# Optimization experiments

Hardware: AMD Instinct MI355X
Metric: run time of the kernel (lower is better)

The kernel has to match this reference:

```python
import jax, jax.numpy as jnp
import numpy as np

B, H, W = 16, 512, 512
NF, EMB, HEADS, NCLS, G = 1024, 768, 12, 4, 16

# segment start indices: RL pts 0:44, LL 44:94, heart 94:120 (groups not connected)
_SEG_STARTS = np.concatenate([np.arange(0, 43), np.arange(44, 93), np.arange(94, 119)])
# num_regions==6 ROI boxes mapped to the 16x16 grid: rows int(b0*16):int(b2*16), cols int(b1*16):int(b3*16)
_BOXES = [(0, 6, 0, 8), (4, 11, 0, 8), (9, 16, 0, 8), (0, 6, 8, 16), (4, 11, 8, 16), (9, 16, 8, 16)]


def _rasterize(landmarks):
    # vectorized replacement of the per-point index_put_/arange loops
    pts = jnp.clip((landmarks * H).astype(jnp.int32), 0, H - 1)   # [B,120,2] (x,y)
    p1 = pts[:, _SEG_STARTS]                                      # [B,S,2]
    p2 = pts[:, _SEG_STARTS + 1]
    k = jnp.arange(H)                                             # max steps per segment
    dy = p2[..., 1] - p1[..., 1]
    dx = p2[..., 0] - p1[..., 0]
    valid = (k < dy[..., None]) & (k < dx[..., None])             # [B,S,K]
    yi = jnp.clip(p1[..., 1:2] + k, 0, H - 1)
    xi = jnp.clip(p1[..., 0:1] + k, 0, W - 1)
    b = jnp.arange(landmarks.shape[0])[:, None, None]
    flat = ((b * H + yi) * W + xi).reshape(-1)
    mask = jnp.zeros(landmarks.shape[0] * H * W, jnp.float32)
    mask = mask.at[flat].max(valid.reshape(-1).astype(jnp.float32))
    return mask.reshape(-1, 1, H, W)


def _affine_grid(theta):
    # torch.nn.functional.affine_grid, align_corners=False
    xs = (2.0 * jnp.arange(W) + 1.0) / W - 1.0
    ys = (2.0 * jnp.arange(H) + 1.0) / H - 1.0
    gx, gy = jnp.meshgrid(xs, ys)                                 # [H,W]
    base = jnp.stack([gx, gy, jnp.ones_like(gx)], -1)             # [H,W,3]
    return jnp.einsum('hwk,bjk->bhwj', base, theta)               # [B,H,W,2]


def _grid_sample(img, grid):
    # bilinear, zero padding, align_corners=False
    Bs, C, Hi, Wi = img.shape
    fx = ((grid[..., 0] + 1.0) * Wi - 1.0) * 0.5
    fy = ((grid[..., 1] + 1.0) * Hi - 1.0) * 0.5
    x0, y0 = jnp.floor(fx), jnp.floor(fy)
    wx1, wy1 = fx - x0, fy - y0
    b = jnp.arange(Bs)[:, None, None]

    def gather(yi, xi):
        ok = (yi >= 0) & (yi < Hi) & (xi >= 0) & (xi < Wi)
        v = img[b, :, jnp.clip(yi, 0, Hi - 1).astype(jnp.int32), jnp.clip(xi, 0, Wi - 1).astype(jnp.int32)]  # [B,H,W,C]
        return v * ok[..., None]

    out = (gather(y0, x0) * ((1 - wy1) * (1 - wx1))[..., None]
           + gather(y0, x0 + 1) * ((1 - wy1) * wx1)[..., None]
           + gather(y0 + 1, x0) * (wy1 * (1 - wx1))[..., None]
           + gather(y0 + 1, x0 + 1) * (wy1 * wx1)[..., None])
    return out.transpose(0, 3, 1, 2)


def _ln(x, g, b):
    m = x.mean(-1, keepdims=True)
    v = ((x - m) ** 2).mean(-1, keepdims=True)
    return (x - m) / jnp.sqrt(v + 1e-5) * g + b


def _pool_rois(x):
    outs = [jax.image.resize(x[:, :, r0:r1, c0:c1], (x.shape[0], x.shape[1], G, G), 'bilinear')
            for r0, r1, c0, c1 in _BOXES]
    return jnp.stack(outs, 1)                                     # [B,6,C,16,16]


def _forward(x, landmarks, stn_w1, stn_b1, stn_w2, stn_b2, conv_w, conv_b, pe_w, pe_b, pos,
             ln1_g, ln1_b, qkv_w, qkv_b, proj_w, proj_b, ln2_g, ln2_b,
             mlp_w1, mlp_b1, mlp_w2, mlp_b2, fc_w, fc_b):
    seg_mask = jax.lax.stop_gradient(_rasterize(landmarks))       # frozen no_grad seg path
    # STN localization: pool mask -> dense(50) -> dense(6) affine theta
    pooled = seg_mask.reshape(B, 1, 32, H // 32, 32, W // 32).mean((3, 5))
    h = jnp.tanh(pooled.reshape(B, -1) @ stn_w1 + stn_b1)
    theta = (h @ stn_w2 + stn_b2).reshape(B, 2, 3)
    grid = _affine_grid(theta)
    transformed_mask = _grid_sample(seg_mask, grid)
    transformed_img = _grid_sample(x, grid)
    # backbone stand-in: stride-32 conv 512->16, num_features=1024
    feat = jax.lax.conv_general_dilated(transformed_img, conv_w, (32, 32), 'VALID')
    feat = jax.nn.relu(feat + conv_b[None, :, None, None])        # [B,NF,16,16]
    tok = feat.reshape(B, NF, G * G).transpose(0, 2, 1) @ pe_w + pe_b + pos
    # one pre-norm transformer encoder block
    t = _ln(tok, ln1_g, ln1_b)
    qkv = (t @ qkv_w + qkv_b).reshape(B, G * G, 3, HEADS, EMB // HEADS)
    q, k, v = qkv[:, :, 0], qkv[:, :, 1], qkv[:, :, 2]
    attn = jax.nn.softmax(jnp.einsum('bqhd,bkhd->bhqk', q, k) / np.sqrt(EMB // HEADS).astype(np.float32), -1)
    o = jnp.einsum('bhqk,bkhd->bqhd', attn, v).reshape(B, G * G, EMB)
    tok = tok + o @ proj_w + proj_b
    t2 = _ln(tok, ln2_g, ln2_b)
    tok = tok + jax.nn.gelu(t2 @ mlp_w1 + mlp_b1) @ mlp_w2 + mlp_b2
    fmap = tok.reshape(B, G, G, EMB).transpose(0, 3, 1, 2)        # [B,768,16,16]
    feats = _pool_rois(fmap).mean((-2, -1))                       # [B,6,768] ROI-GAP
    scores = jax.nn.softmax(feats @ fc_w + fc_b, -1)              # [B,6,4]
    return scores, transformed_img, transformed_mask


def setup_inputs():
    key = jax.random.key(0)
    ks = jax.random.split(key, 12)
    s = 0.02
    return dict(
        x=jax.random.normal(ks[0], (B, 3, H, W), jnp.float32),
        landmarks=jax.random.uniform(ks[1], (B, 120, 2), jnp.float32),
        stn_w1=jax.random.normal(ks[2], (1024, 50), jnp.float32) * s,
        stn_b1=jnp.zeros(50, jnp.float32),
        stn_w2=jax.random.normal(ks[3], (50, 6), jnp.float32) * 0.001,
        stn_b2=jnp.array([1.0, 0.0, 0.0, 0.0, 1.0, 0.0], jnp.float32),
        conv_w=jax.random.normal(ks[4], (NF, 3, 32, 32), jnp.float32) * s,
        conv_b=jnp.zeros(NF, jnp.float32),
        pe_w=jax.random.normal(ks[5], (NF, EMB), jnp.float32) * s,
        pe_b=jnp.zeros(EMB, jnp.float32),
        pos=jax.random.normal(ks[6], (G * G, EMB), jnp.float32) * s,
        ln1_g=jnp.ones(EMB, jnp.float32), ln1_b=jnp.zeros(EMB, jnp.float32),
        qkv_w=jax.random.normal(ks[7], (EMB, 3 * EMB), jnp.float32) * s,
        qkv_b=jnp.zeros(3 * EMB, jnp.float32),
        proj_w=jax.random.normal(ks[8], (EMB, EMB), jnp.float32) * s,
        proj_b=jnp.zeros(EMB, jnp.float32),
        ln2_g=jnp.ones(EMB, jnp.float32), ln2_b=jnp.zeros(EMB, jnp.float32),
        mlp_w1=jax.random.normal(ks[9], (EMB, 4 * EMB), jnp.float32) * s,
        mlp_b1=jnp.zeros(4 * EMB, jnp.float32),
        mlp_w2=jax.random.normal(ks[10], (4 * EMB, EMB), jnp.float32) * s,
        mlp_b2=jnp.zeros(EMB, jnp.float32),
        fc_w=jax.random.normal(ks[11], (EMB, NCLS), jnp.float32) * s,
        fc_b=jnp.zeros(NCLS, jnp.float32),
    )


def reference(x, landmarks, stn_w1, stn_b1, stn_w2, stn_b2, conv_w, conv_b, pe_w, pe_b, pos,
              ln1_g, ln1_b, qkv_w, qkv_b, proj_w, proj_b, ln2_g, ln2_b,
              mlp_w1, mlp_b1, mlp_w2, mlp_b2, fc_w, fc_b):
    return _forward(x, landmarks, stn_w1, stn_b1, stn_w2, stn_b2, conv_w, conv_b, pe_w, pe_b, pos,
                    ln1_g, ln1_b, qkv_w, qkv_b, proj_w, proj_b, ln2_g, ln2_b,
                    mlp_w1, mlp_b1, mlp_w2, mlp_b2, fc_w, fc_b)
```

## Files before the change

kernel.cpp:

```cpp
#include <hip/hip_runtime.h>
#include <hip/hip_bf16.h>
#include <cstdint>


#define B_    16
#define HH    512
#define WW    512
#define NF_   1024
#define EMB_  768
#define HEADS_ 12
#define NTOK  256
#define M_    (B_*NTOK)
#define KCONV 3072

typedef __bf16 bf16_t;
typedef __bf16 bf16x8 __attribute__((ext_vector_type(8)));
typedef float  f32x4  __attribute__((ext_vector_type(4)));

typedef __attribute__((address_space(1))) const void* gas_t;
typedef __attribute__((address_space(3))) void* las_t;

__device__ __forceinline__ void gload16(const bf16_t* g, bf16_t* l) {
    __builtin_amdgcn_global_load_lds((gas_t)g, (las_t)l, 16, 0, 0);
}

__device__ __forceinline__ float tanh_fast(float x) {
    return 1.0f - 2.0f / (__expf(2.0f * x) + 1.0f);
}

__global__ __launch_bounds__(128)
void raster_kernel(const float* __restrict__ lm, float* __restrict__ seg) {
    int b = blockIdx.x;
    int s = threadIdx.x;
    if (s >= 117) return;
    int seg0 = (s < 43) ? s : ((s < 92) ? s + 1 : s + 2);
    const float* p = lm + (size_t)b * 240;
    int p1x = min(max((int)(p[seg0*2 + 0] * 512.0f), 0), 511);
    int p1y = min(max((int)(p[seg0*2 + 1] * 512.0f), 0), 511);
    int p2x = min(max((int)(p[(seg0+1)*2 + 0] * 512.0f), 0), 511);
    int p2y = min(max((int)(p[(seg0+1)*2 + 1] * 512.0f), 0), 511);
    int dy = p2y - p1y, dx = p2x - p1x;
    int kmax = min(dy, dx);
    float* sb = seg + (size_t)b * (HH*WW);
    for (int k = 0; k < kmax; ++k) {
        int yi = min(p1y + k, 511);
        int xi = min(p1x + k, 511);
        sb[yi*WW + xi] = 1.0f;
    }
}

__global__ __launch_bounds__(256)
void pool_kernel(const float* __restrict__ seg, float* __restrict__ pooled) {
    int idx = blockIdx.x * 256 + threadIdx.x;
    int ox = idx & 31, oy = (idx >> 5) & 31, b = idx >> 10;
    const float* sb = seg + (size_t)b * (HH*WW) + (oy*16)*WW + ox*16;
    float s = 0.0f;
    for (int dy = 0; dy < 16; ++dy) {
        #pragma unroll
        for (int dx = 0; dx < 16; ++dx) s += sb[dy*WW + dx];
    }
    pooled[idx] = s * (1.0f/256.0f);
}

__global__ __launch_bounds__(256)
void transpose_w1_kernel(const float* __restrict__ in, float* __restrict__ out) {
    int idx = blockIdx.x * 256 + threadIdx.x;
    int j = idx >> 10, k = idx & 1023;
    out[idx] = in[k*50 + j];
}

__global__ __launch_bounds__(1024)
void stn2_kernel(const float* __restrict__ pooled, const float* __restrict__ w1t,
                 const float* __restrict__ b1, const float* __restrict__ w2,
                 const float* __restrict__ b2, float* __restrict__ theta) {
    __shared__ float pl[1024];
    __shared__ float hl[56];
    int b = blockIdx.x, tid = threadIdx.x;
    pl[tid] = pooled[b*1024 + tid];
    __syncthreads();
    int wave = tid >> 6, lane = tid & 63;
    #pragma unroll
    for (int p = 0; p < 4; ++p) {
        int j = wave + (p << 4);
        if (j < 50) {
            const float* wr = w1t + j*1024;
            float acc = 0.0f;
            #pragma unroll
            for (int i = 0; i < 16; ++i) {
                int k = lane + (i << 6);
                acc = fmaf(pl[k], wr[k], acc);
            }
            #pragma unroll
            for (int off = 32; off; off >>= 1) acc += __shfl_xor(acc, off);
            if (lane == 0) hl[j] = tanhf(acc + b1[j]);
        }
    }
    __syncthreads();
    if (tid < 6) {
        float acc = b2[tid];
        for (int k = 0; k < 50; ++k) acc = fmaf(hl[k], w2[k*6 + tid], acc);
        theta[b*6 + tid] = acc;
    }
}

__global__ __launch_bounds__(256)
void gridsample_kernel(const float* __restrict__ x, const float* __restrict__ seg,
                       const float* __restrict__ theta,
                       float* __restrict__ timg, float* __restrict__ tmask,
                       bf16_t* __restrict__ timgb) {
    size_t idx = (size_t)blockIdx.x * 256 + threadIdx.x;
    int xx = (int)(idx & 511);
    int yy = (int)((idx >> 9) & 511);
    int b  = (int)(idx >> 18);
    __shared__ float th[6];
    if (threadIdx.x < 6) th[threadIdx.x] = theta[b*6 + threadIdx.x];
    __syncthreads();
    float gx = (2.0f*xx + 1.0f) * (1.0f/512.0f) - 1.0f;
    float gy = (2.0f*yy + 1.0f) * (1.0f/512.0f) - 1.0f;
    float g0 = gx*th[0] + gy*th[1] + th[2];
    float g1 = gx*th[3] + gy*th[4] + th[5];
    float fx = ((g0 + 1.0f)*512.0f - 1.0f)*0.5f;
    float fy = ((g1 + 1.0f)*512.0f - 1.0f)*0.5f;
    float x0f = floorf(fx), y0f = floorf(fy);
    float wx1 = fx - x0f,  wy1 = fy - y0f;
    int ix0 = (int)x0f, iy0 = (int)y0f;
    int ix1 = ix0 + 1,  iy1 = iy0 + 1;
    float fy0ok = (iy0 >= 0 && iy0 < HH) ? 1.0f : 0.0f;
    float fy1ok = (iy1 >= 0 && iy1 < HH) ? 1.0f : 0.0f;
    float fx0ok = (ix0 >= 0 && ix0 < WW) ? 1.0f : 0.0f;
    float fx1ok = (ix1 >= 0 && ix1 < WW) ? 1.0f : 0.0f;
    float w00 = (1.0f-wy1)*(1.0f-wx1) * fy0ok * fx0ok;
    float w01 = (1.0f-wy1)*wx1        * fy0ok * fx1ok;
    float w10 = wy1*(1.0f-wx1)        * fy1ok * fx0ok;
    float w11 = wy1*wx1               * fy1ok * fx1ok;
    int cx0 = min(max(ix0,0),511), cx1 = min(max(ix1,0),511);
    int cy0 = min(max(iy0,0),511), cy1 = min(max(iy1,0),511);
    int i00 = cy0*WW + cx0, i01 = cy0*WW + cx1, i10 = cy1*WW + cx0, i11 = cy1*WW + cx1;
    size_t pix = (size_t)yy*WW + xx;
    #pragma unroll
    for (int c = 0; c < 3; ++c) {
        const float* pl = x + ((size_t)(b*3 + c)) * (HH*WW);
        float v = w00*pl[i00] + w01*pl[i01] + w10*pl[i10] + w11*pl[i11];
        timg [((size_t)(b*3 + c))*(HH*WW) + pix] = v;
        timgb[((size_t)(b*3 + c))*(HH*WW) + pix] = (bf16_t)v;
    }
    const float* sp = seg + (size_t)b * (HH*WW);
    float mv = w00*sp[i00] + w01*sp[i01] + w10*sp[i10] + w11*sp[i11];
    tmask[(size_t)b*(HH*WW) + pix] = mv;
}

__global__ __launch_bounds__(256)
void convert_bf16_kernel(const float* __restrict__ in, bf16_t* __restrict__ out) {
    int idx = (blockIdx.x * 256 + threadIdx.x) * 8;
    float4 v0 = *reinterpret_cast<const float4*>(in + idx);
    float4 v1 = *reinterpret_cast<const float4*>(in + idx + 4);
    bf16x8 o;
    o[0]=(bf16_t)v0.x; o[1]=(bf16_t)v0.y; o[2]=(bf16_t)v0.z; o[3]=(bf16_t)v0.w;
    o[4]=(bf16_t)v1.x; o[5]=(bf16_t)v1.y; o[6]=(bf16_t)v1.z; o[7]=(bf16_t)v1.w;
    *reinterpret_cast<bf16x8*>(out + idx) = o;
}

__global__ __launch_bounds__(256)
void transpose_bf16_kernel(const float* __restrict__ in, bf16_t* __restrict__ out,
                           int K, int N) {
    __shared__ float tile[32][33];
    int bk = blockIdx.y * 32, bn = blockIdx.x * 32;
    int r = threadIdx.x >> 5, c = threadIdx.x & 31;
    #pragma unroll
    for (int i = 0; i < 4; ++i)
        tile[r + 8*i][c] = in[(size_t)(bk + r + 8*i) * N + bn + c];
    __syncthreads();
    #pragma unroll
    for (int i = 0; i < 4; ++i)
        out[(size_t)(bn + r + 8*i) * K + bk + c] = (bf16_t)tile[c][r + 8*i];
}

enum { EPI_CONV=0, EPI_PE=1, EPI_QKV=2, EPI_PROJ=3, EPI_GELU=4, EPI_MLP2=5 };

template<int EPI>
__device__ __forceinline__ void gemm_epilogue64(
        f32x4 (&acc)[2][2], const float* bias, const float* extra,
        float* Cf, bf16_t* Cb, int bm, int bn, int wm, int wn,
        int rr, int g, int N) {
    #pragma unroll
    for (int i = 0; i < 2; ++i) {
        #pragma unroll
        for (int j = 0; j < 2; ++j) {
            #pragma unroll
            for (int r = 0; r < 4; ++r) {
                int m = bm + wm + i*16 + g*4 + r;
                int n = bn + wn + j*16 + rr;
                size_t o = (size_t)m * N + n;
                float v = acc[i][j][r] + bias[n];
                if (EPI == EPI_CONV) {
                    Cb[o] = (bf16_t)fmaxf(v, 0.0f);
                } else if (EPI == EPI_PE) {
                    Cf[o] = v + extra[(size_t)(m & 255)*N + n];
                } else if (EPI == EPI_QKV) {
                    Cb[o] = (bf16_t)v;
                } else if (EPI == EPI_PROJ || EPI == EPI_MLP2) {
                    Cf[o] = v + Cf[o];
                } else if (EPI == EPI_GELU) {
                    float u = v;
                    float gl = 0.5f*u*(1.0f + tanh_fast(0.7978845608028654f*(u + 0.044715f*u*u*u)));
                    Cb[o] = (bf16_t)gl;
                }
            }
        }
    }
}

template<int EPI>
__global__ __launch_bounds__(256)
void gemm64_kernel(const bf16_t* __restrict__ A, const bf16_t* __restrict__ Bt,
                   const float* __restrict__ bias, const float* __restrict__ extra,
                   float* __restrict__ Cf, bf16_t* __restrict__ Cb,
                   int M, int N, int K) {
    __shared__ __align__(16) bf16_t As[2][64*64];
    __shared__ __align__(16) bf16_t Bs[2][64*64];
    const int tid = threadIdx.x;
    const int nN   = N >> 6;
    const int nblk = (M >> 6) * nN;
    const int q    = nblk >> 3;
    const int id   = (blockIdx.x & 7) * q + (blockIdx.x >> 3);
    const int bm = (id / nN) * 64, bn = (id % nN) * 64;
    const int lane = tid & 63, w = tid >> 6;
    const int rr = lane & 15, g = lane >> 4;
    const int wm = (w & 1) * 32, wn = (w >> 1) * 32;
    const int sr = tid >> 3;
    const int sc = ((tid & 7) ^ (sr & 7)) * 8;
    const bf16_t* gA0 = A  + (size_t)(bm + sr)      * K + sc;
    const bf16_t* gA1 = A  + (size_t)(bm + 32 + sr) * K + sc;
    const bf16_t* gB0 = Bt + (size_t)(bn + sr)      * K + sc;
    const bf16_t* gB1 = Bt + (size_t)(bn + 32 + sr) * K + sc;

    auto STAGE = [&](int buf, int k0) {
        gload16(gA0 + k0, As[buf] + w*512);
        gload16(gA1 + k0, As[buf] + 2048 + w*512);
        gload16(gB0 + k0, Bs[buf] + w*512);
        gload16(gB1 + k0, Bs[buf] + 2048 + w*512);
    };

    const int s0 = (0*4 + g) ^ (rr & 7);
    const int s1 = (1*4 + g) ^ (rr & 7);

    f32x4 acc[2][2] = {};
    STAGE(0, 0);
    __syncthreads();
    int cur = 0;
    for (int k0 = 0; k0 < K; k0 += 64) {
        if (k0 + 64 < K) STAGE(cur ^ 1, k0 + 64);
        bf16x8 af[2][2], bfv[2][2];
        #pragma unroll
        for (int i = 0; i < 2; ++i) {
            int ra = (wm + i*16 + rr) * 64;
            af[i][0] = *reinterpret_cast<const bf16x8*>(As[cur] + ra + s0*8);
            af[i][1] = *reinterpret_cast<const bf16x8*>(As[cur] + ra + s1*8);
            int rb = (wn + i*16 + rr) * 64;
            bfv[i][0] = *reinterpret_cast<const bf16x8*>(Bs[cur] + rb + s0*8);
            bfv[i][1] = *reinterpret_cast<const bf16x8*>(Bs[cur] + rb + s1*8);
        }
        #pragma unroll
        for (int ks = 0; ks < 2; ++ks)
            #pragma unroll
            for (int i = 0; i < 2; ++i)
                #pragma unroll
                for (int j = 0; j < 2; ++j)
                    acc[i][j] = __builtin_amdgcn_mfma_f32_16x16x32_bf16(
                        af[i][ks], bfv[j][ks], acc[i][j], 0, 0, 0);
        __syncthreads();
        cur ^= 1;
    }
    gemm_epilogue64<EPI>(acc, bias, extra, Cf, Cb, bm, bn, wm, wn, rr, g, N);
}

__global__ __launch_bounds__(256)
void gemm_conv64_kernel(const bf16_t* __restrict__ timgb, const bf16_t* __restrict__ Bt,
                        const float* __restrict__ bias, bf16_t* __restrict__ Cb) {
    const int N = NF_, K = KCONV;
    __shared__ __align__(16) bf16_t As[2][64*64];
    __shared__ __align__(16) bf16_t Bs[2][64*64];
    const int tid = threadIdx.x;
    const int nN   = N >> 6;
    const int nblk = (M_ >> 6) * nN;
    const int q    = nblk >> 3;
    const int id   = (blockIdx.x & 7) * q + (blockIdx.x >> 3);
    const int bm = (id / nN) * 64, bn = (id % nN) * 64;
    const int lane = tid & 63, w = tid >> 6;
    const int rr = lane & 15, g = lane >> 4;
    const int wm = (w & 1) * 32, wn = (w >> 1) * 32;
    const int sr = tid >> 3;
    const int s  = (tid & 7) ^ (sr & 7);
    int row0 = bm + sr, row1 = bm + 32 + sr;
    int b0 = row0 >> 8, py0 = (row0 >> 4) & 15, px0 = row0 & 15;
    int b1 = row1 >> 8, py1 = (row1 >> 4) & 15, px1 = row1 & 15;
    size_t off0 = (size_t)b0*786432 + py0*16384 + px0*32 + (s>>2)*512 + (s&3)*8;
    size_t off1 = (size_t)b1*786432 + py1*16384 + px1*32 + (s>>2)*512 + (s&3)*8;
    const bf16_t* gB0 = Bt + (size_t)(bn + sr)      * K + s*8;
    const bf16_t* gB1 = Bt + (size_t)(bn + 32 + sr) * K + s*8;

    auto STAGE = [&](int buf, int k0) {
        int c   = k0 >> 10;
        int ky0 = (k0 >> 5) & 31;
        size_t koff = (size_t)c*262144 + (size_t)ky0*512;
        gload16(timgb + off0 + koff, As[buf] + w*512);
        gload16(timgb + off1 + koff, As[buf] + 2048 + w*512);
        gload16(gB0 + k0, Bs[buf] + w*512);
        gload16(gB1 + k0, Bs[buf] + 2048 + w*512);
    };

    const int s0 = (0*4 + g) ^ (rr & 7);
    const int s1 = (1*4 + g) ^ (rr & 7);

    f32x4 acc[2][2] = {};
    STAGE(0, 0);
    __syncthreads();
    int cur = 0;
    for (int k0 = 0; k0 < K; k0 += 64) {
        if (k0 + 64 < K) STAGE(cur ^ 1, k0 + 64);
        bf16x8 af[2][2], bfv[2][2];
        #pragma unroll
        for (int i = 0; i < 2; ++i) {
            int ra = (wm + i*16 + rr) * 64;
            af[i][0] = *reinterpret_cast<const bf16x8*>(As[cur] + ra + s0*8);
            af[i][1] = *reinterpret_cast<const bf16x8*>(As[cur] + ra + s1*8);
            int rb = (wn + i*16 + rr) * 64;
            bfv[i][0] = *reinterpret_cast<const bf16x8*>(Bs[cur] + rb + s0*8);
            bfv[i][1] = *reinterpret_cast<const bf16x8*>(Bs[cur] + rb + s1*8);
        }
        #pragma unroll
        for (int ks = 0; ks < 2; ++ks)
            #pragma unroll
            for (int i = 0; i < 2; ++i)
                #pragma unroll
                for (int j = 0; j < 2; ++j)
                    acc[i][j] = __builtin_amdgcn_mfma_f32_16x16x32_bf16(
                        af[i][ks], bfv[j][ks], acc[i][j], 0, 0, 0);
        __syncthreads();
        cur ^= 1;
    }
    gemm_epilogue64<EPI_CONV>(acc, bias, nullptr, nullptr, Cb, bm, bn, wm, wn, rr, g, N);
}

__global__ __launch_bounds__(256)
void ln_kernel(const float* __restrict__ x, const float* __restrict__ g,
               const float* __restrict__ be, bf16_t* __restrict__ out) {
    int r = blockIdx.x, tid = threadIdx.x;
    const float* xr = x + (size_t)r * EMB_;
    float v0 = xr[tid], v1 = xr[tid+256], v2 = xr[tid+512];
    float s = v0+v1+v2, s2 = v0*v0 + v1*v1 + v2*v2;
    __shared__ float red[8];
    #pragma unroll
    for (int off = 32; off; off >>= 1) { s += __shfl_xor(s, off); s2 += __shfl_xor(s2, off); }
    if ((tid & 63) == 0) { red[tid>>6] = s; red[4 + (tid>>6)] = s2; }
    __syncthreads();
    s  = red[0]+red[1]+red[2]+red[3];
    s2 = red[4]+red[5]+red[6]+red[7];
    float mean = s * (1.0f/768.0f);
    float var  = s2 * (1.0f/768.0f) - mean*mean;
    float rstd = rsqrtf(var + 1e-5f);
    bf16_t* orow = out + (size_t)r * EMB_;
    orow[tid]     = (bf16_t)((v0-mean)*rstd*g[tid]     + be[tid]);
    orow[tid+256] = (bf16_t)((v1-mean)*rstd*g[tid+256] + be[tid+256]);
    orow[tid+512] = (bf16_t)((v2-mean)*rstd*g[tid+512] + be[tid+512]);
}

__global__ __launch_bounds__(256)
void attn_kernel5(const bf16_t* __restrict__ qkv, bf16_t* __restrict__ o) {
    __shared__ __align__(16) bf16_t Ks[256*72];
    __shared__ __align__(16) bf16_t Vt[64*264];
    __shared__ __align__(16) bf16_t Ps[4][64*72];
    const int tid  = threadIdx.x;
    const int lane = tid & 63, w = tid >> 6;
    const int rr   = lane & 15, g = lane >> 4;
    const int h = blockIdx.x % HEADS_;
    const int b = blockIdx.x / HEADS_;
    const bf16_t* base = qkv + (size_t)(b*256)*2304;

    {
        const bf16_t* kr = base + (size_t)tid*2304 + 768  + h*64;
        const bf16_t* vr = base + (size_t)tid*2304 + 1536 + h*64;
        bf16_t* kd = Ks + tid*72;
        #pragma unroll
        for (int c2 = 0; c2 < 8; ++c2) {
            *reinterpret_cast<bf16x8*>(kd + c2*8) =
                *reinterpret_cast<const bf16x8*>(kr + c2*8);
            bf16x8 v = *reinterpret_cast<const bf16x8*>(vr + c2*8);
            #pragma unroll
            for (int e = 0; e < 8; ++e)
                Vt[(c2*8 + e)*264 + tid] = v[e];
        }
    }

    bf16x8 qf[4][2];
    #pragma unroll
    for (int i = 0; i < 4; ++i)
        #pragma unroll
        for (int ks = 0; ks < 2; ++ks)
            qf[i][ks] = *reinterpret_cast<const bf16x8*>(
                base + (size_t)(w*64 + i*16 + rr)*2304 + h*64 + ks*32 + g*8);

    f32x4 oacc[4][4] = {};
    float lacc[4][4] = {};
    __syncthreads();

    bf16_t* Pw = Ps[w];
    for (int kc = 0; kc < 4; ++kc) {
        f32x4 sacc[4][4] = {};
        #pragma unroll
        for (int ks = 0; ks < 2; ++ks) {
            bf16x8 kf[4];
            #pragma unroll
            for (int j = 0; j < 4; ++j)
                kf[j] = *reinterpret_cast<const bf16x8*>(
                    Ks + (size_t)(kc*64 + j*16 + rr)*72 + ks*32 + g*8);
            #pragma unroll
            for (int i = 0; i < 4; ++i)
                #pragma unroll
                for (int j = 0; j < 4; ++j)
                    sacc[i][j] = __builtin_amdgcn_mfma_f32_16x16x32_bf16(
                        qf[i][ks], kf[j], sacc[i][j], 0, 0, 0);
        }
        #pragma unroll
        for (int i = 0; i < 4; ++i) {
            #pragma unroll
            for (int r = 0; r < 4; ++r) {
                int prow = i*16 + g*4 + r;
                float ps = 0.0f;
                #pragma unroll
                for (int j = 0; j < 4; ++j) {
                    float p = __expf(sacc[i][j][r] * 0.125f);
                    ps += p;
                    Pw[prow*72 + j*16 + rr] = (bf16_t)p;
                }
                lacc[i][r] += ps;
            }
        }
        #pragma unroll
        for (int ks = 0; ks < 2; ++ks) {
            bf16x8 pa[4], vb[4];
            #pragma unroll
            for (int i = 0; i < 4; ++i)
                pa[i] = *reinterpret_cast<const bf16x8*>(
                    Pw + (size_t)(i*16 + rr)*72 + ks*32 + g*8);
            #pragma unroll
            for (int n = 0; n < 4; ++n)
                vb[n] = *reinterpret_cast<const bf16x8*>(
                    Vt + (size_t)(n*16 + rr)*264 + kc*64 + ks*32 + g*8);
            #pragma unroll
            for (int i = 0; i < 4; ++i)
                #pragma unroll
                for (int n = 0; n < 4; ++n)
                    oacc[i][n] = __builtin_amdgcn_mfma_f32_16x16x32_bf16(
                        pa[i], vb[n], oacc[i][n], 0, 0, 0);
        }
    }

    #pragma unroll
    for (int i = 0; i < 4; ++i) {
        #pragma unroll
        for (int r = 0; r < 4; ++r) {
            float v = lacc[i][r];
            v += __shfl_xor(v, 1);
            v += __shfl_xor(v, 2);
            v += __shfl_xor(v, 4);
            v += __shfl_xor(v, 8);
            lacc[i][r] = 1.0f / v;
        }
    }
    #pragma unroll
    for (int i = 0; i < 4; ++i) {
        #pragma unroll
        for (int r = 0; r < 4; ++r) {
            int qrow = w*64 + i*16 + g*4 + r;
            bf16_t* orow = o + (size_t)(b*256 + qrow)*EMB_ + h*64;
            float inv = lacc[i][r];
            #pragma unroll
            for (int n = 0; n < 4; ++n)
                orow[n*16 + rr] = (bf16_t)(oacc[i][n][r] * inv);
        }
    }
}

__global__ __launch_bounds__(256)
void head_feats_kernel(const float* __restrict__ tok, float* __restrict__ feats) {
    const int bx[6][4] = {{0,6,0,8},{4,11,0,8},{9,16,0,8},{0,6,8,16},{4,11,8,16},{9,16,8,16}};
    int chunk = blockIdx.x % 3;
    int box   = (blockIdx.x / 3) % 6;
    int b     = blockIdx.x / 18;
    int r0 = bx[box][0], r1 = bx[box][1], c0 = bx[box][2], c1 = bx[box][3];
    int rh = r1 - r0, rw = c1 - c0;
    __shared__ float wl[256];
    int tid = threadIdx.x;
    int py = tid >> 4, px = tid & 15;
    float w = 0.0f;
    if (py >= r0 && py < r1 && px >= c0 && px < c1) {
        int ly = py - r0, lx = px - c0;
        float cy = 0.0f, cx = 0.0f;
        for (int o = 0; o < 16; ++o) {
            float sy = (o + 0.5f) * (float)rh * (1.0f/16.0f) - 0.5f;
            sy = fminf(fmaxf(sy, 0.0f), (float)(rh - 1));
            int i0 = (int)floorf(sy); float t = sy - (float)i0;
            if (ly == i0)     cy += 1.0f - t;
            if (ly == i0 + 1) cy += t;
            float sx = (o + 0.5f) * (float)rw * (1.0f/16.0f) - 0.5f;
            sx = fminf(fmaxf(sx, 0.0f), (float)(rw - 1));
            int j0 = (int)floorf(sx); float u = sx - (float)j0;
            if (lx == j0)     cx += 1.0f - u;
            if (lx == j0 + 1) cx += u;
        }
        w = (cy * (1.0f/16.0f)) * (cx * (1.0f/16.0f));
    }
    wl[tid] = w;
    __syncthreads();
    int e = chunk*256 + tid;
    float f = 0.0f;
    for (int iy = r0; iy < r1; ++iy)
        for (int ix = c0; ix < c1; ++ix) {
            int p = iy*16 + ix;
            f = fmaf(wl[p], tok[((size_t)(b*256 + p))*EMB_ + e], f);
        }
    feats[(size_t)(b*6 + box)*EMB_ + e] = f;
}

__global__ __launch_bounds__(256)
void head_logits_kernel(const float* __restrict__ feats, const float* __restrict__ fcw,
                        const float* __restrict__ fcb, float* __restrict__ scores) {
    int tid = threadIdx.x;
    const float* fr = feats + (size_t)blockIdx.x * EMB_;
    __shared__ float red[4];
    float lg[4];
    #pragma unroll
    for (int cc = 0; cc < 4; ++cc) {
        float part = 0.0f;
        for (int e = tid; e < EMB_; e += 256) part = fmaf(fr[e], fcw[e*4 + cc], part);
        #pragma unroll
        for (int off = 32; off; off >>= 1) part += __shfl_xor(part, off);
        __syncthreads();
        if ((tid & 63) == 0) red[tid>>6] = part;
        __syncthreads();
        lg[cc] = red[0]+red[1]+red[2]+red[3] + fcb[cc];
    }
    if (tid == 0) {
        float mx = fmaxf(fmaxf(lg[0],lg[1]), fmaxf(lg[2],lg[3]));
        float e0 = expf(lg[0]-mx), e1 = expf(lg[1]-mx), e2 = expf(lg[2]-mx), e3 = expf(lg[3]-mx);
        float inv = 1.0f/(e0+e1+e2+e3);
        float* out = scores + (size_t)blockIdx.x * 4;
        out[0] = e0*inv; out[1] = e1*inv; out[2] = e2*inv; out[3] = e3*inv;
    }
}

extern "C" void kernel_launch(void* const* d_in, const int* in_sizes, int n_in,
                              void* d_out, int out_size, void* d_ws, size_t ws_size,
                              hipStream_t stream) {
    (void)in_sizes; (void)n_in; (void)out_size; (void)ws_size;
    const float* x       = (const float*)d_in[0];
    const float* lm      = (const float*)d_in[1];
    const float* stn_w1  = (const float*)d_in[2];
    const float* stn_b1  = (const float*)d_in[3];
    const float* stn_w2  = (const float*)d_in[4];
    const float* stn_b2  = (const float*)d_in[5];
    const float* conv_w  = (const float*)d_in[6];
    const float* conv_b  = (const float*)d_in[7];
    const float* pe_w    = (const float*)d_in[8];
    const float* pe_b    = (const float*)d_in[9];
    const float* pos     = (const float*)d_in[10];
    const float* ln1_g   = (const float*)d_in[11];
    const float* ln1_b   = (const float*)d_in[12];
    const float* qkv_w   = (const float*)d_in[13];
    const float* qkv_b   = (const float*)d_in[14];
    const float* proj_w  = (const float*)d_in[15];
    const float* proj_b  = (const float*)d_in[16];
    const float* ln2_g   = (const float*)d_in[17];
    const float* ln2_b   = (const float*)d_in[18];
    const float* mlp_w1  = (const float*)d_in[19];
    const float* mlp_b1  = (const float*)d_in[20];
    const float* mlp_w2  = (const float*)d_in[21];
    const float* mlp_b2  = (const float*)d_in[22];
    const float* fc_w    = (const float*)d_in[23];
    const float* fc_b    = (const float*)d_in[24];

    float* out    = (float*)d_out;
    float* scores = out;
    float* timg   = out + 384;
    float* tmask  = out + 384 + (size_t)B_*3*HH*WW;

    char* ws = (char*)d_ws;
    size_t off = 0;
    auto alloc = [&](size_t bytes) {
        off = (off + 255) & ~(size_t)255;
        void* p = ws + off; off += bytes; return p;
    };
    char*   slotBig = (char*)alloc(25165824);
    char*   slotT   = (char*)alloc((size_t)B_*3*HH*WW*2);
    char*   slotC   = (char*)alloc((size_t)M_*NF_*2);
    float*  tok     = (float*)alloc((size_t)M_*EMB_*4);
    bf16_t* tbuf    = (bf16_t*)alloc((size_t)M_*EMB_*2);
    bf16_t* conv_wb = (bf16_t*)alloc((size_t)NF_*KCONV*2);
    bf16_t* pe_wb   = (bf16_t*)alloc((size_t)EMB_*NF_*2);
    bf16_t* qkv_wb  = (bf16_t*)alloc((size_t)3*EMB_*EMB_*2);
    bf16_t* proj_wb = (bf16_t*)alloc((size_t)EMB_*EMB_*2);
    bf16_t* mlp1_wb = (bf16_t*)alloc((size_t)4*EMB_*EMB_*2);
    bf16_t* mlp2_wb = (bf16_t*)alloc((size_t)EMB_*4*EMB_*2);
    float*  w1t     = (float*)alloc(50*1024*4);
    float*  pooled  = (float*)alloc(16384*4);
    float*  theta   = (float*)alloc(96*4);
    float*  feats   = (float*)alloc((size_t)B_*6*EMB_*4);

    float*  seg    = (float*)slotBig;
    bf16_t* hidden = (bf16_t*)slotBig;
    bf16_t* timgb  = (bf16_t*)slotT;
    bf16_t* qkvb   = (bf16_t*)slotT;
    bf16_t* featC  = (bf16_t*)slotC;
    bf16_t* obuf   = (bf16_t*)slotC;

    convert_bf16_kernel<<<(NF_*KCONV)/8/256, 256, 0, stream>>>(conv_w, conv_wb);
    transpose_bf16_kernel<<<dim3(EMB_/32, NF_/32),    256, 0, stream>>>(pe_w,   pe_wb,   NF_,  EMB_);
    transpose_bf16_kernel<<<dim3(3*EMB_/32, EMB_/32), 256, 0, stream>>>(qkv_w,  qkv_wb,  EMB_, 3*EMB_);
    transpose_bf16_kernel<<<dim3(EMB_/32, EMB_/32),   256, 0, stream>>>(proj_w, proj_wb, EMB_, EMB_);
    transpose_bf16_kernel<<<dim3(4*EMB_/32, EMB_/32), 256, 0, stream>>>(mlp_w1, mlp1_wb, EMB_, 4*EMB_);
    transpose_bf16_kernel<<<dim3(EMB_/32, 4*EMB_/32), 256, 0, stream>>>(mlp_w2, mlp2_wb, 4*EMB_, EMB_);
    transpose_w1_kernel<<<200, 256, 0, stream>>>(stn_w1, w1t);

    hipMemsetAsync(seg, 0, (size_t)B_*HH*WW*sizeof(float), stream);
    raster_kernel<<<B_, 128, 0, stream>>>(lm, seg);
    pool_kernel<<<64, 256, 0, stream>>>(seg, pooled);
    stn2_kernel<<<B_, 1024, 0, stream>>>(pooled, w1t, stn_b1, stn_w2, stn_b2, theta);
    gridsample_kernel<<<(B_*HH*WW)/256, 256, 0, stream>>>(x, seg, theta, timg, tmask, timgb);

    gemm_conv64_kernel<<<(M_/64)*(NF_/64), 256, 0, stream>>>(
        timgb, conv_wb, conv_b, featC);

    gemm64_kernel<EPI_PE><<<(M_/64)*(EMB_/64), 256, 0, stream>>>(
        featC, pe_wb, pe_b, pos, tok, nullptr, M_, EMB_, NF_);

    ln_kernel<<<M_, 256, 0, stream>>>(tok, ln1_g, ln1_b, tbuf);
    gemm64_kernel<EPI_QKV><<<(M_/64)*(3*EMB_/64), 256, 0, stream>>>(
        tbuf, qkv_wb, qkv_b, nullptr, nullptr, qkvb, M_, 3*EMB_, EMB_);

    attn_kernel5<<<B_*HEADS_, 256, 0, stream>>>(qkvb, obuf);

    gemm64_kernel<EPI_PROJ><<<(M_/64)*(EMB_/64), 256, 0, stream>>>(
        obuf, proj_wb, proj_b, nullptr, tok, nullptr, M_, EMB_, EMB_);

    ln_kernel<<<M_, 256, 0, stream>>>(tok, ln2_g, ln2_b, tbuf);
    gemm64_kernel<EPI_GELU><<<(M_/64)*(4*EMB_/64), 256, 0, stream>>>(
        tbuf, mlp1_wb, mlp_b1, nullptr, nullptr, hidden, M_, 4*EMB_, EMB_);
    gemm64_kernel<EPI_MLP2><<<(M_/64)*(EMB_/64), 256, 0, stream>>>(
        hidden, mlp2_wb, mlp_b2, nullptr, tok, nullptr, M_, EMB_, 4*EMB_);

    head_feats_kernel<<<B_*6*3, 256, 0, stream>>>(tok, feats);
    head_logits_kernel<<<B_*6, 256, 0, stream>>>(feats, fc_w, fc_b, scores);
}
```

Measured before the change: 311.0 us.

## Enlarge GEMM tiles to 128xBN with K-step 32 for higher operand reuse

All GEMMs, including the implicit-im2col conv GEMM, move from 64x64 tiles with K-step 64 to 128x128 or 128x64 tiles with K-step 32. Each wave now computes a 64xBN/2 sub-tile with 4xFJ MFMAs per step, and the LDS swizzle is reworked for 32-wide rows. The aim is more MFMA work per LDS and global load and less global traffic per output. In exchange there are fewer blocks (for example 256 for the conv GEMM), more accumulator registers and twice as many K-loop barriers.

```diff
diff --git a/kernel.cpp b/kernel.cpp
--- a/kernel.cpp
+++ b/kernel.cpp
@@ -177,15 +177,15 @@
 
 enum { EPI_CONV=0, EPI_PE=1, EPI_QKV=2, EPI_PROJ=3, EPI_GELU=4, EPI_MLP2=5 };
 
-template<int EPI>
-__device__ __forceinline__ void gemm_epilogue64(
-        f32x4 (&acc)[2][2], const float* bias, const float* extra,
+template<int EPI, int FJ>
+__device__ __forceinline__ void gemm_epilogue128(
+        f32x4 (&acc)[4][FJ], const float* bias, const float* extra,
         float* Cf, bf16_t* Cb, int bm, int bn, int wm, int wn,
         int rr, int g, int N) {
     #pragma unroll
-    for (int i = 0; i < 2; ++i) {
-        #pragma unroll
-        for (int j = 0; j < 2; ++j) {
+    for (int i = 0; i < 4; ++i) {
+        #pragma unroll
+        for (int j = 0; j < FJ; ++j) {
             #pragma unroll
             for (int r = 0; r < 4; ++r) {
                 int m = bm + wm + i*16 + g*4 + r;
@@ -210,136 +210,125 @@
     }
 }
 
-template<int EPI>
-__global__ __launch_bounds__(256)
-void gemm64_kernel(const bf16_t* __restrict__ A, const bf16_t* __restrict__ Bt,
-                   const float* __restrict__ bias, const float* __restrict__ extra,
-                   float* __restrict__ Cf, bf16_t* __restrict__ Cb,
-                   int M, int N, int K) {
-    __shared__ __align__(16) bf16_t As[2][64*64];
-    __shared__ __align__(16) bf16_t Bs[2][64*64];
+template<int EPI, int BN>
+__global__ __launch_bounds__(256)
+void gemm128_kernel(const bf16_t* __restrict__ A, const bf16_t* __restrict__ Bt,
+                    const float* __restrict__ bias, const float* __restrict__ extra,
+                    float* __restrict__ Cf, bf16_t* __restrict__ Cb,
+                    int M, int N, int K) {
+    constexpr int FJ = BN / 32;
+    __shared__ __align__(16) bf16_t As[2][128*32];
+    __shared__ __align__(16) bf16_t Bs[2][BN*32];
     const int tid = threadIdx.x;
-    const int nN   = N >> 6;
-    const int nblk = (M >> 6) * nN;
+    const int nN   = N / BN;
+    const int nblk = (M >> 7) * nN;
     const int q    = nblk >> 3;
     const int id   = (blockIdx.x & 7) * q + (blockIdx.x >> 3);
-    const int bm = (id / nN) * 64, bn = (id % nN) * 64;
+    const int bm = (id / nN) * 128, bn = (id % nN) * BN;
     const int lane = tid & 63, w = tid >> 6;
     const int rr = lane & 15, g = lane >> 4;
-    const int wm = (w & 1) * 32, wn = (w >> 1) * 32;
-    const int sr = tid >> 3;
-    const int sc = ((tid & 7) ^ (sr & 7)) * 8;
-    const bf16_t* gA0 = A  + (size_t)(bm + sr)      * K + sc;
-    const bf16_t* gA1 = A  + (size_t)(bm + 32 + sr) * K + sc;
-    const bf16_t* gB0 = Bt + (size_t)(bn + sr)      * K + sc;
-    const bf16_t* gB1 = Bt + (size_t)(bn + 32 + sr) * K + sc;
+    const int wm = (w & 1) * 64, wn = (w >> 1) * (BN/2);
+
+    const int arow  = tid >> 2;
+    const int aslot = ((tid & 3) ^ (arow & 3)) * 8;
+    const bf16_t* gA0 = A  + (size_t)(bm + arow) * K + aslot;
+    const bf16_t* gA1 = gA0 + (size_t)64 * K;
+    const bf16_t* gB0 = Bt + (size_t)(bn + arow) * K + aslot;
+    const bf16_t* gB1 = gB0 + (size_t)64 * K;
 
     auto STAGE = [&](int buf, int k0) {
         gload16(gA0 + k0, As[buf] + w*512);
         gload16(gA1 + k0, As[buf] + 2048 + w*512);
         gload16(gB0 + k0, Bs[buf] + w*512);
-        gload16(gB1 + k0, Bs[buf] + 2048 + w*512);
+        if (BN == 128)
+            gload16(gB1 + k0, Bs[buf] + 2048 + w*512);
     };
 
-    const int s0 = (0*4 + g) ^ (rr & 7);
-    const int s1 = (1*4 + g) ^ (rr & 7);
-
-    f32x4 acc[2][2] = {};
+    const int rs = (g ^ (rr & 3)) * 8;
+
+    f32x4 acc[4][FJ] = {};
     STAGE(0, 0);
     __syncthreads();
     int cur = 0;
-    for (int k0 = 0; k0 < K; k0 += 64) {
-        if (k0 + 64 < K) STAGE(cur ^ 1, k0 + 64);
-        bf16x8 af[2][2], bfv[2][2];
-        #pragma unroll
-        for (int i = 0; i < 2; ++i) {
-            int ra = (wm + i*16 + rr) * 64;
-            af[i][0] = *reinterpret_cast<const bf16x8*>(As[cur] + ra + s0*8);
-            af[i][1] = *reinterpret_cast<const bf16x8*>(As[cur] + ra + s1*8);
-            int rb = (wn + i*16 + rr) * 64;
-            bfv[i][0] = *reinterpret_cast<const bf16x8*>(Bs[cur] + rb + s0*8);
-            bfv[i][1] = *reinterpret_cast<const bf16x8*>(Bs[cur] + rb + s1*8);
-        }
-        #pragma unroll
-        for (int ks = 0; ks < 2; ++ks)
-            #pragma unroll
-            for (int i = 0; i < 2; ++i)
-                #pragma unroll
-                for (int j = 0; j < 2; ++j)
-                    acc[i][j] = __builtin_amdgcn_mfma_f32_16x16x32_bf16(
-                        af[i][ks], bfv[j][ks], acc[i][j], 0, 0, 0);
+    for (int k0 = 0; k0 < K; k0 += 32) {
+        if (k0 + 32 < K) STAGE(cur ^ 1, k0 + 32);
+        bf16x8 af[4], bfv[FJ];
+        #pragma unroll
+        for (int i = 0; i < 4; ++i)
+            af[i] = *reinterpret_cast<const bf16x8*>(As[cur] + (wm + i*16 + rr)*32 + rs);
+        #pragma unroll
+        for (int j = 0; j < FJ; ++j)
+            bfv[j] = *reinterpret_cast<const bf16x8*>(Bs[cur] + (wn + j*16 + rr)*32 + rs);
+        #pragma unroll
+        for (int i = 0; i < 4; ++i)
+            #pragma unroll
+            for (int j = 0; j < FJ; ++j)
+                acc[i][j] = __builtin_amdgcn_mfma_f32_16x16x32_bf16(af[i], bfv[j], acc[i][j], 0, 0, 0);
         __syncthreads();
         cur ^= 1;
     }
-    gemm_epilogue64<EPI>(acc, bias, extra, Cf, Cb, bm, bn, wm, wn, rr, g, N);
-}
-
-__global__ __launch_bounds__(256)
-void gemm_conv64_kernel(const bf16_t* __restrict__ timgb, const bf16_t* __restrict__ Bt,
-                        const float* __restrict__ bias, bf16_t* __restrict__ Cb) {
+    gemm_epilogue128<EPI, FJ>(acc, bias, extra, Cf, Cb, bm, bn, wm, wn, rr, g, N);
+}
+
+__global__ __launch_bounds__(256)
+void gemm_conv128_kernel(const bf16_t* __restrict__ timgb, const bf16_t* __restrict__ Bt,
+                         const float* __restrict__ bias, bf16_t* __restrict__ Cb) {
+    constexpr int BN = 128, FJ = 4;
     const int N = NF_, K = KCONV;
-    __shared__ __align__(16) bf16_t As[2][64*64];
-    __shared__ __align__(16) bf16_t Bs[2][64*64];
+    __shared__ __align__(16) bf16_t As[2][128*32];
+    __shared__ __align__(16) bf16_t Bs[2][BN*32];
     const int tid = threadIdx.x;
-    const int nN   = N >> 6;
-    const int nblk = (M_ >> 6) * nN;
+    const int nN   = N / BN;
+    const int nblk = (M_ >> 7) * nN;
     const int q    = nblk >> 3;
     const int id   = (blockIdx.x & 7) * q + (blockIdx.x >> 3);
-    const int bm = (id / nN) * 64, bn = (id % nN) * 64;
+    const int bm = (id / nN) * 128, bn = (id % nN) * BN;
     const int lane = tid & 63, w = tid >> 6;
     const int rr = lane & 15, g = lane >> 4;
-    const int wm = (w & 1) * 32, wn = (w >> 1) * 32;
-    const int sr = tid >> 3;
-    const int s  = (tid & 7) ^ (sr & 7);
-    int row0 = bm + sr, row1 = bm + 32 + sr;
+    const int wm = (w & 1) * 64, wn = (w >> 1) * (BN/2);
+
+    const int arow  = tid >> 2;
+    const int aslot = ((tid & 3) ^ (arow & 3)) * 8;
+    int row0 = bm + arow, row1 = row0 + 64;
     int b0 = row0 >> 8, py0 = (row0 >> 4) & 15, px0 = row0 & 15;
     int b1 = row1 >> 8, py1 = (row1 >> 4) & 15, px1 = row1 & 15;
-    size_t off0 = (size_t)b0*786432 + py0*16384 + px0*32 + (s>>2)*512 + (s&3)*8;
-    size_t off1 = (size_t)b1*786432 + py1*16384 + px1*32 + (s>>2)*512 + (s&3)*8;
-    const bf16_t* gB0 = Bt + (size_t)(bn + sr)      * K + s*8;
-    const bf16_t* gB1 = Bt + (size_t)(bn + 32 + sr) * K + s*8;
+    size_t off0 = (size_t)b0*786432 + py0*16384 + px0*32 + aslot;
+    size_t off1 = (size_t)b1*786432 + py1*16384 + px1*32 + aslot;
+    const bf16_t* gB0 = Bt + (size_t)(bn + arow) * K + aslot;
+    const bf16_t* gB1 = gB0 + (size_t)64 * K;
 
     auto STAGE = [&](int buf, int k0) {
-        int c   = k0 >> 10;
-        int ky0 = (k0 >> 5) & 31;
-        size_t koff = (size_t)c*262144 + (size_t)ky0*512;
+        size_t koff = (size_t)(k0 >> 10)*262144 + (size_t)((k0 >> 5) & 31)*512;
         gload16(timgb + off0 + koff, As[buf] + w*512);
         gload16(timgb + off1 + koff, As[buf] + 2048 + w*512);
         gload16(gB0 + k0, Bs[buf] + w*512);
         gload16(gB1 + k0, Bs[buf] + 2048 + w*512);
     };
 
-    const int s0 = (0*4 + g) ^ (rr & 7);
-    const int s1 = (1*4 + g) ^ (rr & 7);
-
-    f32x4 acc[2][2] = {};
+    const int rs = (g ^ (rr & 3)) * 8;
+
+    f32x4 acc[4][FJ] = {};
     STAGE(0, 0);
     __syncthreads();
     int cur = 0;
-    for (int k0 = 0; k0 < K; k0 += 64) {
-        if (k0 + 64 < K) STAGE(cur ^ 1, k0 + 64);
-        bf16x8 af[2][2], bfv[2][2];
-        #pragma unroll
-        for (int i = 0; i < 2; ++i) {
-            int ra = (wm + i*16 + rr) * 64;
-            af[i][0] = *reinterpret_cast<const bf16x8*>(As[cur] + ra + s0*8);
-            af[i][1] = *reinterpret_cast<const bf16x8*>(As[cur] + ra + s1*8);
-            int rb = (wn + i*16 + rr) * 64;
-            bfv[i][0] = *reinterpret_cast<const bf16x8*>(Bs[cur] + rb + s0*8);
-            bfv[i][1] = *reinterpret_cast<const bf16x8*>(Bs[cur] + rb + s1*8);
-        }
-        #pragma unroll
-        for (int ks = 0; ks < 2; ++ks)
-            #pragma unroll
-            for (int i = 0; i < 2; ++i)
-                #pragma unroll
-                for (int j = 0; j < 2; ++j)
-                    acc[i][j] = __builtin_amdgcn_mfma_f32_16x16x32_bf16(
-                        af[i][ks], bfv[j][ks], acc[i][j], 0, 0, 0);
+    for (int k0 = 0; k0 < K; k0 += 32) {
+        if (k0 + 32 < K) STAGE(cur ^ 1, k0 + 32);
+        bf16x8 af[4], bfv[FJ];
+        #pragma unroll
+        for (int i = 0; i < 4; ++i)
+            af[i] = *reinterpret_cast<const bf16x8*>(As[cur] + (wm + i*16 + rr)*32 + rs);
+        #pragma unroll
+        for (int j = 0; j < FJ; ++j)
+            bfv[j] = *reinterpret_cast<const bf16x8*>(Bs[cur] + (wn + j*16 + rr)*32 + rs);
+        #pragma unroll
+        for (int i = 0; i < 4; ++i)
+            #pragma unroll
+            for (int j = 0; j < FJ; ++j)
+                acc[i][j] = __builtin_amdgcn_mfma_f32_16x16x32_bf16(af[i], bfv[j], acc[i][j], 0, 0, 0);
         __syncthreads();
         cur ^= 1;
     }
-    gemm_epilogue64<EPI_CONV>(acc, bias, nullptr, nullptr, Cb, bm, bn, wm, wn, rr, g, N);
+    gemm_epilogue128<EPI_CONV, FJ>(acc, bias, nullptr, nullptr, Cb, bm, bn, wm, wn, rr, g, N);
 }
 
 __global__ __launch_bounds__(256)
@@ -628,25 +617,25 @@
     stn2_kernel<<<B_, 1024, 0, stream>>>(pooled, w1t, stn_b1, stn_w2, stn_b2, theta);
     gridsample_kernel<<<(B_*HH*WW)/256, 256, 0, stream>>>(x, seg, theta, timg, tmask, timgb);
 
-    gemm_conv64_kernel<<<(M_/64)*(NF_/64), 256, 0, stream>>>(
+    gemm_conv128_kernel<<<(M_/128)*(NF_/128), 256, 0, stream>>>(
         timgb, conv_wb, conv_b, featC);
 
-    gemm64_kernel<EPI_PE><<<(M_/64)*(EMB_/64), 256, 0, stream>>>(
+    gemm128_kernel<EPI_PE, 64><<<(M_/128)*(EMB_/64), 256, 0, stream>>>(
         featC, pe_wb, pe_b, pos, tok, nullptr, M_, EMB_, NF_);
 
     ln_kernel<<<M_, 256, 0, stream>>>(tok, ln1_g, ln1_b, tbuf);
-    gemm64_kernel<EPI_QKV><<<(M_/64)*(3*EMB_/64), 256, 0, stream>>>(
+    gemm128_kernel<EPI_QKV, 128><<<(M_/128)*(3*EMB_/128), 256, 0, stream>>>(
         tbuf, qkv_wb, qkv_b, nullptr, nullptr, qkvb, M_, 3*EMB_, EMB_);
 
     attn_kernel5<<<B_*HEADS_, 256, 0, stream>>>(qkvb, obuf);
 
-    gemm64_kernel<EPI_PROJ><<<(M_/64)*(EMB_/64), 256, 0, stream>>>(
+    gemm128_kernel<EPI_PROJ, 64><<<(M_/128)*(EMB_/64), 256, 0, stream>>>(
         obuf, proj_wb, proj_b, nullptr, tok, nullptr, M_, EMB_, EMB_);
 
     ln_kernel<<<M_, 256, 0, stream>>>(tok, ln2_g, ln2_b, tbuf);
-    gemm64_kernel<EPI_GELU><<<(M_/64)*(4*EMB_/64), 256, 0, stream>>>(
+    gemm128_kernel<EPI_GELU, 128><<<(M_/128)*(4*EMB_/128), 256, 0, stream>>>(
         tbuf, mlp1_wb, mlp_b1, nullptr, nullptr, hidden, M_, 4*EMB_, EMB_);
-    gemm64_kernel<EPI_MLP2><<<(M_/64)*(EMB_/64), 256, 0, stream>>>(
+    gemm128_kernel<EPI_MLP2, 64><<<(M_/128)*(EMB_/64), 256, 0, stream>>>(
         hidden, mlp2_wb, mlp_b2, nullptr, tok, nullptr, M_, EMB_, 4*EMB_);
 
     head_feats_kernel<<<B_*6*3, 256, 0, stream>>>(tok, feats);
```

Result: slower. 370.4 us (+19.1%).
